# Optimization experiments

Measured on AMD Instinct MI355X. Metric: run time of the kernel, lower is better.

## Reference

```python
import jax, jax.numpy as jnp
import numpy as np

N = 50000
E = 800000
EPS = 1e-12


def sage_conv(x, src, dst, W_l, b_l, W_r):
    # PyG SAGEConv (mean aggr): out = lin_l(mean_{j in N(i)} x_j) + lin_r(x_i)
    msg = x[src]                                             # [E, d] gather
    agg = jax.ops.segment_sum(msg, dst, num_segments=N)      # [N, d]
    cnt = jax.ops.segment_sum(jnp.ones((E,), x.dtype), dst, num_segments=N)
    mean = agg / jnp.maximum(cnt, 1.0)[:, None]              # isolated nodes -> 0
    return mean @ W_l + b_l + x @ W_r


def setup_inputs() -> dict:
    key = jax.random.key(0)
    ks = jax.random.split(key, 12)
    s = 0.05
    return {
        "x": jax.random.normal(ks[0], (N, 128), dtype=jnp.float32),
        "edge_index": jax.random.randint(ks[1], (2, E), 0, N, dtype=jnp.int64),
        # pre: Linear(128 -> 128)
        "pre_W": jax.random.normal(ks[2], (128, 128), dtype=jnp.float32) * s,
        "pre_b": jnp.zeros((128,), dtype=jnp.float32),
        # conv_first: SAGEConv(128 -> 256)
        "W1_l": jax.random.normal(ks[3], (128, 256), dtype=jnp.float32) * s,
        "b1": jnp.zeros((256,), dtype=jnp.float32),
        "W1_r": jax.random.normal(ks[4], (128, 256), dtype=jnp.float32) * s,
        # conv_hidden[0]: SAGEConv(256 -> 256)
        "W2_l": jax.random.normal(ks[5], (256, 256), dtype=jnp.float32) * s,
        "b2": jnp.zeros((256,), dtype=jnp.float32),
        "W2_r": jax.random.normal(ks[6], (256, 256), dtype=jnp.float32) * s,
        # conv_out: SAGEConv(256 -> 256)
        "W3_l": jax.random.normal(ks[7], (256, 256), dtype=jnp.float32) * s,
        "b3": jnp.zeros((256,), dtype=jnp.float32),
        "W3_r": jax.random.normal(ks[8], (256, 256), dtype=jnp.float32) * s,
    }


def reference(x, edge_index, pre_W, pre_b, W1_l, b1, W1_r, W2_l, b2, W2_r, W3_l, b3, W3_r):
    src, dst = edge_index[0], edge_index[1]
    h = x @ pre_W + pre_b                                   # feature_pre Linear
    h = jax.nn.relu(sage_conv(h, src, dst, W1_l, b1, W1_r))  # dropout = identity (eval)
    h = jax.nn.relu(sage_conv(h, src, dst, W2_l, b2, W2_r))
    h = sage_conv(h, src, dst, W3_l, b3, W3_r)
    norm = jnp.sqrt(jnp.sum(h * h, axis=-1, keepdims=True))
    return h / jnp.maximum(norm, EPS)                       # F.normalize(p=2, dim=-1)
```

## Files before the change

### kernel.cpp

```cpp
#include <hip/hip_runtime.h>
#include <cstddef>
#include <cstdint>


typedef __attribute__((ext_vector_type(8))) short short8;
typedef __attribute__((ext_vector_type(4))) float f32x4;
typedef __attribute__((ext_vector_type(2))) float f32x2;

__device__ __forceinline__ unsigned rne_bf16(float f) {
    unsigned b = __float_as_uint(f);
    return (b + 0x7fffu + ((b >> 16) & 1u)) >> 16;
}
__device__ __forceinline__ float bf16_lo(unsigned u) { return __uint_as_float(u << 16); }
__device__ __forceinline__ float bf16_hi(unsigned u) { return __uint_as_float(u & 0xffff0000u); }


__device__ __forceinline__ float dec_e4m3_sw(unsigned v) {
    unsigned s = (v & 0x80u) << 24;
    unsigned em = v & 0x7fu;
    float out;
    if (em < 8u) {
        out = (float)em * 0.001953125f;
    } else {
        out = __uint_as_float((((em >> 3) + 120u) << 23) | ((em & 7u) << 20));
    }
    return __uint_as_float(__float_as_uint(out) | s);
}

__device__ __forceinline__ unsigned char enc_e4m3(float f) {
#if __has_builtin(__builtin_amdgcn_cvt_pk_fp8_f32)
    return (unsigned char)(__builtin_amdgcn_cvt_pk_fp8_f32(f, f, 0, false) & 0xff);
#else
    unsigned b = __float_as_uint(f);
    unsigned s = (b >> 24) & 0x80u;
    unsigned a = b & 0x7fffffffu;
    if (a >= 0x43E00000u) return (unsigned char)(s | 0x7Eu);
    if (a < 0x3C800000u) {
        unsigned m = (unsigned)rintf(__uint_as_float(a) * 512.0f);
        return (unsigned char)(s | m);
    }
    unsigned r = a + 0x7FFFFu + ((a >> 20) & 1u);
    unsigned E8 = (r >> 23) - 120u;
    unsigned M = (r >> 20) & 7u;
    if (E8 > 15u || (E8 == 15u && M == 7u)) return (unsigned char)(s | 0x7Eu);
    return (unsigned char)(s | (E8 << 3) | M);
#endif
}

__device__ __forceinline__ void acc16(float* a, uint4 u) {
#if __has_builtin(__builtin_amdgcn_cvt_pk_f32_fp8)
    f32x2 f;
    f = __builtin_amdgcn_cvt_pk_f32_fp8(u.x, false); a[0] += f.x;  a[1] += f.y;
    f = __builtin_amdgcn_cvt_pk_f32_fp8(u.x, true);  a[2] += f.x;  a[3] += f.y;
    f = __builtin_amdgcn_cvt_pk_f32_fp8(u.y, false); a[4] += f.x;  a[5] += f.y;
    f = __builtin_amdgcn_cvt_pk_f32_fp8(u.y, true);  a[6] += f.x;  a[7] += f.y;
    f = __builtin_amdgcn_cvt_pk_f32_fp8(u.z, false); a[8] += f.x;  a[9] += f.y;
    f = __builtin_amdgcn_cvt_pk_f32_fp8(u.z, true);  a[10] += f.x; a[11] += f.y;
    f = __builtin_amdgcn_cvt_pk_f32_fp8(u.w, false); a[12] += f.x; a[13] += f.y;
    f = __builtin_amdgcn_cvt_pk_f32_fp8(u.w, true);  a[14] += f.x; a[15] += f.y;
#else
    unsigned d0 = u.x, d1 = u.y, d2 = u.z, d3 = u.w;
#pragma unroll
    for (int t = 0; t < 4; ++t) a[t]      += dec_e4m3_sw((d0 >> (8 * t)) & 0xffu);
#pragma unroll
    for (int t = 0; t < 4; ++t) a[4 + t]  += dec_e4m3_sw((d1 >> (8 * t)) & 0xffu);
#pragma unroll
    for (int t = 0; t < 4; ++t) a[8 + t]  += dec_e4m3_sw((d2 >> (8 * t)) & 0xffu);
#pragma unroll
    for (int t = 0; t < 4; ++t) a[12 + t] += dec_e4m3_sw((d3 >> (8 * t)) & 0xffu);
#endif
}

__device__ __forceinline__ void stage16(const void* g, unsigned short* ldsbase,
                                        int lane) {
#if __has_builtin(__builtin_amdgcn_global_load_lds)
    (void)lane;
    __builtin_amdgcn_global_load_lds(
        (const __attribute__((address_space(1))) unsigned int*)g,
        (__attribute__((address_space(3))) unsigned int*)ldsbase, 16, 0, 0);
#else
    *(uint4*)(ldsbase + (size_t)lane * 8) = *(const uint4*)g;
#endif
}


__global__ __launch_bounds__(256) void deg_kernel(const int* __restrict__ dst,
                                                  int* __restrict__ deg, int E) {
    int e = blockIdx.x * 256 + threadIdx.x;
    if (e < E) atomicAdd(&deg[dst[e]], 1);
}

__global__ __launch_bounds__(256) void bsum_kernel(const int* __restrict__ deg,
                                                   int* __restrict__ bsum, int n) {
    int i = blockIdx.x * 256 + threadIdx.x;
    int v = (i < n) ? deg[i] : 0;
#pragma unroll
    for (int s = 32; s > 0; s >>= 1) v += __shfl_down(v, s);
    __shared__ int ws[4];
    int lane = threadIdx.x & 63, w = threadIdx.x >> 6;
    if (lane == 0) ws[w] = v;
    __syncthreads();
    if (threadIdx.x == 0) bsum[blockIdx.x] = ws[0] + ws[1] + ws[2] + ws[3];
}

__global__ __launch_bounds__(256) void bscan_kernel(const int* __restrict__ bsum,
                                                    int* __restrict__ boff,
                                                    int* __restrict__ off,
                                                    int nb, int n, int E) {
    int t = threadIdx.x;
    int v = (t < nb) ? bsum[t] : 0;
    int incl = v;
#pragma unroll
    for (int s = 1; s < 64; s <<= 1) {
        int u = __shfl_up(incl, s);
        if ((t & 63) >= s) incl += u;
    }
    __shared__ int ws[4];
    int lane = t & 63, w = t >> 6;
    if (lane == 63) ws[w] = incl;
    __syncthreads();
    int woff = 0;
    for (int j = 0; j < w; ++j) woff += ws[j];
    if (t < nb) boff[t] = woff + incl - v;
    if (t == 0) off[n] = E;
}

__global__ __launch_bounds__(256) void scan_kernel(const int* __restrict__ deg,
                                                   const int* __restrict__ boff,
                                                   int* __restrict__ off,
                                                   float* __restrict__ inv, int n) {
    int i = blockIdx.x * 256 + threadIdx.x;
    int v = (i < n) ? deg[i] : 0;
    int incl = v;
#pragma unroll
    for (int s = 1; s < 64; s <<= 1) {
        int u = __shfl_up(incl, s);
        if ((threadIdx.x & 63) >= s) incl += u;
    }
    __shared__ int ws[4];
    int lane = threadIdx.x & 63, w = threadIdx.x >> 6;
    if (lane == 63) ws[w] = incl;
    __syncthreads();
    int woff = 0;
    for (int j = 0; j < w; ++j) woff += ws[j];
    if (i < n) {
        off[i] = boff[blockIdx.x] + woff + incl - v;
        inv[i] = 1.0f / fmaxf((float)v, 1.0f);
    }
}

__global__ __launch_bounds__(256) void fill_kernel(const int* __restrict__ src,
                                                   const int* __restrict__ dst,
                                                   const int* __restrict__ off,
                                                   int* __restrict__ deg,
                                                   int* __restrict__ ssrc, int E) {
    int e = blockIdx.x * 256 + threadIdx.x;
    if (e >= E) return;
    int d = dst[e];
    int pos = off[d] + atomicSub(&deg[d], 1) - 1;
    ssrc[pos] = src[e];
}


__global__ __launch_bounds__(256) void prep_all(
    const float* __restrict__ x, uint2* __restrict__ xb, int n4, int XB,
    const float* __restrict__ pre_W, const float* __restrict__ W1_l,
    const float* __restrict__ W1_r, const float* __restrict__ W2_l,
    const float* __restrict__ W2_r, const float* __restrict__ W3_l,
    const float* __restrict__ W3_r,
    unsigned short* __restrict__ WT0, unsigned short* __restrict__ WT1,
    unsigned short* __restrict__ WT2, unsigned short* __restrict__ WT3,
    unsigned short* __restrict__ WT4, unsigned short* __restrict__ WT5,
    unsigned short* __restrict__ WT6) {
    if (blockIdx.x < (unsigned)XB) {
        int i = blockIdx.x * 256 + threadIdx.x;
        if (i >= n4) return;
        float4 v = ((const float4*)x)[i];
        uint2 o;
        o.x = rne_bf16(v.x) | (rne_bf16(v.y) << 16);
        o.y = rne_bf16(v.z) | (rne_bf16(v.w) << 16);
        xb[i] = o;
        return;
    }
    int idx = (blockIdx.x - XB) * 256 + threadIdx.x;
    if (idx < 16384) {
        int k = idx >> 7, n = idx & 127;
        WT0[n * 128 + k] = (unsigned short)rne_bf16(pre_W[idx]);
        return;
    }
    idx -= 16384;
    if (idx < 32768) {
        int k = idx >> 8, n = idx & 255;
        WT1[n * 128 + k] = (unsigned short)rne_bf16(W1_l[idx]);
        return;
    }
    idx -= 32768;
    if (idx < 32768) {
        int k = idx >> 8, n = idx & 255;
        WT2[n * 128 + k] = (unsigned short)rne_bf16(W1_r[idx]);
        return;
    }
    idx -= 32768;
    if (idx < 65536) {
        int k = idx >> 8, n = idx & 255;
        WT3[n * 256 + k] = (unsigned short)rne_bf16(W2_l[idx]);
        return;
    }
    idx -= 65536;
    if (idx < 65536) {
        int k = idx >> 8, n = idx & 255;
        WT4[n * 256 + k] = (unsigned short)rne_bf16(W2_r[idx]);
        return;
    }
    idx -= 65536;
    if (idx < 65536) {
        int k = idx >> 8, n = idx & 255;
        WT5[n * 256 + k] = (unsigned short)rne_bf16(W3_l[idx]);
        return;
    }
    idx -= 65536;
    if (idx < 65536) {
        int k = idx >> 8, n = idx & 255;
        WT6[n * 256 + k] = (unsigned short)rne_bf16(W3_r[idx]);
    }
}


template <int D>
__global__ __launch_bounds__(256) void gather_b(const unsigned short* __restrict__ h,
                                                const int* __restrict__ off,
                                                const int* __restrict__ ssrc,
                                                const float* __restrict__ inv,
                                                unsigned short* __restrict__ agg, int n) {
    int node = blockIdx.x * 4 + (threadIdx.x >> 6);
    if (node >= n) return;
    int lane = threadIdx.x & 63;
    int beg = off[node], end = off[node + 1];
    float sc = inv[node];

    const int q   = lane >> 4;
    const int sub = lane & 15;
    const unsigned short* col = h + (sub << 3);
    float a[8] = {0, 0, 0, 0, 0, 0, 0, 0};
    float b[8] = {0, 0, 0, 0, 0, 0, 0, 0};
    int k = beg;
    for (; k + 7 < end; k += 8) {
        int s0 = ssrc[k + q];
        int s1 = ssrc[k + 4 + q];
        uint4 u = *(const uint4*)(col + (size_t)s0 * D);
        uint4 v = *(const uint4*)(col + (size_t)s1 * D);
        a[0] += bf16_lo(u.x); a[1] += bf16_hi(u.x);
        a[2] += bf16_lo(u.y); a[3] += bf16_hi(u.y);
        a[4] += bf16_lo(u.z); a[5] += bf16_hi(u.z);
        a[6] += bf16_lo(u.w); a[7] += bf16_hi(u.w);
        b[0] += bf16_lo(v.x); b[1] += bf16_hi(v.x);
        b[2] += bf16_lo(v.y); b[3] += bf16_hi(v.y);
        b[4] += bf16_lo(v.z); b[5] += bf16_hi(v.z);
        b[6] += bf16_lo(v.w); b[7] += bf16_hi(v.w);
    }
    for (; k < end; k += 4) {
        int e = k + q;
        if (e < end) {
            uint4 u = *(const uint4*)(col + (size_t)ssrc[e] * D);
            a[0] += bf16_lo(u.x); a[1] += bf16_hi(u.x);
            a[2] += bf16_lo(u.y); a[3] += bf16_hi(u.y);
            a[4] += bf16_lo(u.z); a[5] += bf16_hi(u.z);
            a[6] += bf16_lo(u.w); a[7] += bf16_hi(u.w);
        }
    }
#pragma unroll
    for (int i = 0; i < 8; ++i) a[i] += b[i];
#pragma unroll
    for (int i = 0; i < 8; ++i) a[i] += __shfl_xor(a[i], 16);
#pragma unroll
    for (int i = 0; i < 8; ++i) a[i] += __shfl_xor(a[i], 32);
    if (q == 0) {
#pragma unroll
        for (int i = 0; i < 8; ++i) a[i] *= sc;
        uint4 o;
        o.x = rne_bf16(a[0]) | (rne_bf16(a[1]) << 16);
        o.y = rne_bf16(a[2]) | (rne_bf16(a[3]) << 16);
        o.z = rne_bf16(a[4]) | (rne_bf16(a[5]) << 16);
        o.w = rne_bf16(a[6]) | (rne_bf16(a[7]) << 16);
        *(uint4*)(agg + (size_t)node * D + (sub << 3)) = o;
    }
}


__global__ __launch_bounds__(256) void gather8(const unsigned char* __restrict__ h8,
                                               const int* __restrict__ off,
                                               const int* __restrict__ ssrc,
                                               const float* __restrict__ inv,
                                               unsigned short* __restrict__ agg, int n) {
    int node = blockIdx.x * 4 + (threadIdx.x >> 6);
    if (node >= n) return;
    int lane = threadIdx.x & 63;
    const int q   = lane >> 4;
    const int sub = lane & 15;
    int beg = off[node], end = off[node + 1];
    float sc = inv[node];
    const unsigned char* col = h8 + (sub << 4);

    float a[16], b[16];
#pragma unroll
    for (int i = 0; i < 16; ++i) { a[i] = 0.f; b[i] = 0.f; }

    int k = beg;
    for (; k + 7 < end; k += 8) {
        int s0 = ssrc[k + q];
        int s1 = ssrc[k + 4 + q];
        uint4 u = *(const uint4*)(col + (size_t)s0 * 256);
        uint4 v = *(const uint4*)(col + (size_t)s1 * 256);
        acc16(a, u);
        acc16(b, v);
    }
    for (; k < end; k += 4) {
        int e = k + q;
        if (e < end) {
            uint4 u = *(const uint4*)(col + (size_t)ssrc[e] * 256);
            acc16(a, u);
        }
    }
#pragma unroll
    for (int i = 0; i < 16; ++i) a[i] += b[i];
#pragma unroll
    for (int i = 0; i < 16; ++i) a[i] += __shfl_xor(a[i], 16);
#pragma unroll
    for (int i = 0; i < 16; ++i) a[i] += __shfl_xor(a[i], 32);
    if (q == 0) {
#pragma unroll
        for (int i = 0; i < 16; ++i) a[i] *= sc;
        uint4 o1, o2;
        o1.x = rne_bf16(a[0])  | (rne_bf16(a[1])  << 16);
        o1.y = rne_bf16(a[2])  | (rne_bf16(a[3])  << 16);
        o1.z = rne_bf16(a[4])  | (rne_bf16(a[5])  << 16);
        o1.w = rne_bf16(a[6])  | (rne_bf16(a[7])  << 16);
        o2.x = rne_bf16(a[8])  | (rne_bf16(a[9])  << 16);
        o2.y = rne_bf16(a[10]) | (rne_bf16(a[11]) << 16);
        o2.z = rne_bf16(a[12]) | (rne_bf16(a[13]) << 16);
        o2.w = rne_bf16(a[14]) | (rne_bf16(a[15]) << 16);
        *(uint4*)(agg + (size_t)node * 256 + (sub << 4)) = o1;
        *(uint4*)(agg + (size_t)node * 256 + (sub << 4) + 8) = o2;
    }
}

__global__ __launch_bounds__(256) void gemm_bt(
    const unsigned short* __restrict__ A1, const unsigned short* __restrict__ W1T,
    const float* __restrict__ bias, unsigned short* __restrict__ outb,
    int M, int K, int Nn) {
    __shared__ __align__(16) unsigned short As[128 * 64];
    __shared__ __align__(16) unsigned short Bs[128 * 64];

    const int t = threadIdx.x;
    const int lane = t & 63;
    const int w = t >> 6;
    const int wm = w >> 1, wn = w & 1;
    const int m0 = blockIdx.x * 128;
    const int n0 = blockIdx.y * 128;

    f32x4 acc[4][4];
#pragma unroll
    for (int i = 0; i < 4; ++i)
#pragma unroll
        for (int j = 0; j < 4; ++j) acc[i][j] = (f32x4){0.f, 0.f, 0.f, 0.f};

    for (int k0 = 0; k0 < K; k0 += 64) {
#pragma unroll
        for (int r = 0; r < 4; ++r) {
            int p = r * 256 + t;
            int row = p >> 3, slot = p & 7;
            int c = slot ^ (row & 7);
            int gm = m0 + row;
            if (gm >= M) gm = M - 1;
            uint4 va = *(const uint4*)(A1 + (size_t)gm * K + k0 + c * 8);
            uint4 vb = *(const uint4*)(W1T + (size_t)(n0 + row) * K + k0 + c * 8);
            *(uint4*)&As[(size_t)p * 8] = va;
            *(uint4*)&Bs[(size_t)p * 8] = vb;
        }
        __syncthreads();
#pragma unroll
        for (int kk = 0; kk < 2; ++kk) {
            short8 af[4], bfr[4];
            int ac = kk * 4 + (lane >> 4);
#pragma unroll
            for (int i = 0; i < 4; ++i) {
                int arow = wm * 64 + i * 16 + (lane & 15);
                af[i] = *(const short8*)&As[arow * 64 + ((ac ^ (arow & 7)) << 3)];
                int brow = wn * 64 + i * 16 + (lane & 15);
                bfr[i] = *(const short8*)&Bs[brow * 64 + ((ac ^ (brow & 7)) << 3)];
            }
#pragma unroll
            for (int mi = 0; mi < 4; ++mi)
#pragma unroll
                for (int ni = 0; ni < 4; ++ni)
                    acc[mi][ni] = __builtin_amdgcn_mfma_f32_16x16x32_bf16(
                        af[mi], bfr[ni], acc[mi][ni], 0, 0, 0);
        }
        __syncthreads();
    }

#pragma unroll
    for (int ni = 0; ni < 4; ++ni) {
        int n = n0 + wn * 64 + ni * 16 + (lane & 15);
        float bv = (bias != nullptr) ? bias[n] : 0.0f;
#pragma unroll
        for (int mi = 0; mi < 4; ++mi) {
            int mbase = m0 + wm * 64 + mi * 16 + ((lane >> 4) << 2);
#pragma unroll
            for (int r = 0; r < 4; ++r) {
                int m = mbase + r;
                if (m >= M) continue;
                outb[(size_t)m * Nn + n] = (unsigned short)rne_bf16(acc[mi][ni][r] + bv);
            }
        }
    }
}

__global__ __launch_bounds__(512) void gemm_wide(
    const unsigned short* __restrict__ A1, const unsigned short* __restrict__ W1T,
    const unsigned short* __restrict__ A2, const unsigned short* __restrict__ W2T,
    const float* __restrict__ bias,
    unsigned short* __restrict__ outb, unsigned char* __restrict__ out8,
    float* __restrict__ outf, int M, int K, int relu) {
    __shared__ __align__(16) unsigned short As[128 * 64];
    __shared__ __align__(16) unsigned short Bs[256 * 64];
    __shared__ float rs[128][4];

    const int t = threadIdx.x;
    const int lane = t & 63;
    const int w8 = t >> 6;
    const int wm = w8 >> 2, wn = w8 & 3;
    const int m0 = blockIdx.x * 128;

    f32x4 acc[4][4];
#pragma unroll
    for (int i = 0; i < 4; ++i)
#pragma unroll
        for (int j = 0; j < 4; ++j) acc[i][j] = (f32x4){0.f, 0.f, 0.f, 0.f};

    for (int pass = 0; pass < 2; ++pass) {
        const unsigned short* A = pass ? A2 : A1;
        const unsigned short* W = pass ? W2T : W1T;

        for (int k0 = 0; k0 < K; k0 += 64) {
#pragma unroll
            for (int i = 0; i < 2; ++i) {
                int base = (w8 * 2 + i) * 64;
                int p = base + lane;
                int row = p >> 3, slot = p & 7;
                int c = slot ^ (row & 7);
                int gm = m0 + row;
                if (gm >= M) gm = M - 1;
                stage16(A + (size_t)gm * K + k0 + c * 8, &As[(size_t)base * 8], lane);
            }
#pragma unroll
            for (int i = 0; i < 4; ++i) {
                int base = (w8 * 4 + i) * 64;
                int p = base + lane;
                int row = p >> 3, slot = p & 7;
                int c = slot ^ (row & 7);
                stage16(W + (size_t)row * K + k0 + c * 8, &Bs[(size_t)base * 8], lane);
            }
            __syncthreads();
#pragma unroll
            for (int kk = 0; kk < 2; ++kk) {
                short8 af[4], bfr[4];
                int ac = kk * 4 + (lane >> 4);
#pragma unroll
                for (int i = 0; i < 4; ++i) {
                    int arow = wm * 64 + i * 16 + (lane & 15);
                    af[i] = *(const short8*)&As[arow * 64 + ((ac ^ (arow & 7)) << 3)];
                    int brow = wn * 64 + i * 16 + (lane & 15);
                    bfr[i] = *(const short8*)&Bs[brow * 64 + ((ac ^ (brow & 7)) << 3)];
                }
#pragma unroll
                for (int mi = 0; mi < 4; ++mi)
#pragma unroll
                    for (int ni = 0; ni < 4; ++ni)
                        acc[mi][ni] = __builtin_amdgcn_mfma_f32_16x16x32_bf16(
                            af[mi], bfr[ni], acc[mi][ni], 0, 0, 0);
            }
            __syncthreads();
        }
    }

    if (outb) {
#pragma unroll
        for (int ni = 0; ni < 4; ++ni) {
            int n = wn * 64 + ni * 16 + (lane & 15);
            float bv = bias[n];
#pragma unroll
            for (int mi = 0; mi < 4; ++mi) {
                int mbase = m0 + wm * 64 + mi * 16 + ((lane >> 4) << 2);
#pragma unroll
                for (int r = 0; r < 4; ++r) {
                    int m = mbase + r;
                    if (m >= M) continue;
                    float v = acc[mi][ni][r] + bv;
                    if (relu) v = fmaxf(v, 0.0f);
                    outb[(size_t)m * 256 + n] = (unsigned short)rne_bf16(v);
                    if (out8) out8[(size_t)m * 256 + n] = enc_e4m3(v);
                }
            }
        }
        return;
    }

#pragma unroll
    for (int ni = 0; ni < 4; ++ni) {
        float bv = bias[wn * 64 + ni * 16 + (lane & 15)];
#pragma unroll
        for (int mi = 0; mi < 4; ++mi)
#pragma unroll
            for (int r = 0; r < 4; ++r) acc[mi][ni][r] += bv;
    }
#pragma unroll
    for (int mi = 0; mi < 4; ++mi) {
#pragma unroll
        for (int r = 0; r < 4; ++r) {
            float p = acc[mi][0][r] * acc[mi][0][r] + acc[mi][1][r] * acc[mi][1][r] +
                      acc[mi][2][r] * acc[mi][2][r] + acc[mi][3][r] * acc[mi][3][r];
            p += __shfl_xor(p, 1);
            p += __shfl_xor(p, 2);
            p += __shfl_xor(p, 4);
            p += __shfl_xor(p, 8);
            if ((lane & 15) == 0)
                rs[wm * 64 + mi * 16 + ((lane >> 4) << 2) + r][wn] = p;
        }
    }
    __syncthreads();
#pragma unroll
    for (int mi = 0; mi < 4; ++mi) {
        int mbase = m0 + wm * 64 + mi * 16 + ((lane >> 4) << 2);
        int lrow = wm * 64 + mi * 16 + ((lane >> 4) << 2);
#pragma unroll
        for (int r = 0; r < 4; ++r) {
            int m = mbase + r;
            if (m >= M) continue;
            float s = rs[lrow + r][0] + rs[lrow + r][1] + rs[lrow + r][2] + rs[lrow + r][3];
            float sc = 1.0f / fmaxf(sqrtf(s), 1e-12f);
#pragma unroll
            for (int ni = 0; ni < 4; ++ni) {
                int n = wn * 64 + ni * 16 + (lane & 15);
                outf[(size_t)m * 256 + n] = acc[mi][ni][r] * sc;
            }
        }
    }
}

extern "C" void kernel_launch(void* const* d_in, const int* in_sizes, int n_in,
                              void* d_out, int out_size, void* d_ws, size_t ws_size,
                              hipStream_t stream) {
    const int N = 50000;
    const int E = 800000;
    const int NB = (N + 255) / 256;

    const float* x     = (const float*)d_in[0];
    const int*   ei    = (const int*)d_in[1];
    const float* pre_W = (const float*)d_in[2];
    const float* pre_b = (const float*)d_in[3];
    const float* W1_l  = (const float*)d_in[4];
    const float* b1    = (const float*)d_in[5];
    const float* W1_r  = (const float*)d_in[6];
    const float* W2_l  = (const float*)d_in[7];
    const float* b2    = (const float*)d_in[8];
    const float* W2_r  = (const float*)d_in[9];
    const float* W3_l  = (const float*)d_in[10];
    const float* b3    = (const float*)d_in[11];
    const float* W3_r  = (const float*)d_in[12];
    float* out = (float*)d_out;

    const int* src = ei;
    const int* dst = ei + E;

    int* deg  = (int*)d_ws;
    int* off  = deg + N;
    int* bsum = off + N + 1;
    int* boff = bsum + 256;
    int* ssrc = boff + 256;
    size_t int_words = (size_t)2 * N + 1 + 512 + E;
    int_words = (int_words + 3) & ~(size_t)3;

    float* inv = (float*)d_ws + int_words;
    unsigned short* us = (unsigned short*)(inv + N);

    unsigned short* xb  = us;                 us += (size_t)N * 128;
    unsigned short* WT0 = us;                 us += 16384;
    unsigned short* WT1 = us;                 us += 32768;
    unsigned short* WT2 = us;                 us += 32768;
    unsigned short* WT3 = us;                 us += 65536;
    unsigned short* WT4 = us;                 us += 65536;
    unsigned short* WT5 = us;                 us += 65536;
    unsigned short* WT6 = us;                 us += 65536;
    unsigned short* h0b   = us;               us += (size_t)N * 128;
    unsigned short* agg1b = us;               us += (size_t)N * 128;
    unsigned short* h1b   = us;               us += (size_t)N * 256;
    unsigned short* agg2b = us;               us += (size_t)N * 256;
    unsigned short* h2b   = us;               us += (size_t)N * 256;
    unsigned short* agg3b = us;               us += (size_t)N * 256;
    unsigned char* h1f8 = (unsigned char*)us;
    unsigned char* h2f8 = h1f8 + (size_t)N * 256;

    hipMemsetAsync(deg, 0, (size_t)N * sizeof(int), stream);
    deg_kernel<<<(E + 255) / 256, 256, 0, stream>>>(dst, deg, E);
    bsum_kernel<<<NB, 256, 0, stream>>>(deg, bsum, N);
    bscan_kernel<<<1, 256, 0, stream>>>(bsum, boff, off, NB, N, E);
    scan_kernel<<<NB, 256, 0, stream>>>(deg, boff, off, inv, N);
    fill_kernel<<<(E + 255) / 256, 256, 0, stream>>>(src, dst, off, deg, ssrc, E);

    const int n4 = N * 128 / 4;
    const int XB = (n4 + 255) / 256;
    const int WB = (344064 + 255) / 256;
    prep_all<<<XB + WB, 256, 0, stream>>>(x, (uint2*)xb, n4, XB,
                                          pre_W, W1_l, W1_r, W2_l, W2_r, W3_l,
                                          W3_r, WT0, WT1, WT2, WT3, WT4, WT5, WT6);

    const int MT = (N + 127) / 128;
    const int AG = (N + 3) / 4;

    gemm_bt<<<dim3(MT, 1), 256, 0, stream>>>(xb, WT0, pre_b, h0b, N, 128, 128);

    gather_b<128><<<AG, 256, 0, stream>>>(h0b, off, ssrc, inv, agg1b, N);
    gemm_wide<<<MT, 512, 0, stream>>>(agg1b, WT1, h0b, WT2, b1,
                                      h1b, h1f8, nullptr, N, 128, 1);

    gather8<<<AG, 256, 0, stream>>>(h1f8, off, ssrc, inv, agg2b, N);
    gemm_wide<<<MT, 512, 0, stream>>>(agg2b, WT3, h1b, WT4, b2,
                                      h2b, h2f8, nullptr, N, 256, 1);

    gather8<<<AG, 256, 0, stream>>>(h2f8, off, ssrc, inv, agg3b, N);
    gemm_wide<<<MT, 512, 0, stream>>>(agg3b, WT5, h2b, WT6, b3,
                                      nullptr, nullptr, out, N, 256, 0);
}
```

Baseline: 470.4 us.

## Fuse CSR fill into pre-GEMM launch and halve gemm_wide row tile

```diff
diff --git a/kernel.cpp b/kernel.cpp
--- a/kernel.cpp
+++ b/kernel.cpp
@@ -147,18 +147,6 @@
         off[i] = boff[blockIdx.x] + woff + incl - v;
         inv[i] = 1.0f / fmaxf((float)v, 1.0f);
     }
-}
-
-__global__ __launch_bounds__(256) void fill_kernel(const int* __restrict__ src,
-                                                   const int* __restrict__ dst,
-                                                   const int* __restrict__ off,
-                                                   int* __restrict__ deg,
-                                                   int* __restrict__ ssrc, int E) {
-    int e = blockIdx.x * 256 + threadIdx.x;
-    if (e >= E) return;
-    int d = dst[e];
-    int pos = off[d] + atomicSub(&deg[d], 1) - 1;
-    ssrc[pos] = src[e];
 }
 
 
@@ -344,19 +332,32 @@
     }
 }
 
-__global__ __launch_bounds__(256) void gemm_bt(
-    const unsigned short* __restrict__ A1, const unsigned short* __restrict__ W1T,
-    const float* __restrict__ bias, unsigned short* __restrict__ outb,
-    int M, int K, int Nn) {
+
+__global__ __launch_bounds__(256) void fatB(
+    const unsigned short* __restrict__ xb, const unsigned short* __restrict__ WT0,
+    const float* __restrict__ pre_b, unsigned short* __restrict__ h0b, int M,
+    int GB,
+    const int* __restrict__ src, const int* __restrict__ dst,
+    const int* __restrict__ off, int* __restrict__ deg,
+    int* __restrict__ ssrc, int E) {
     __shared__ __align__(16) unsigned short As[128 * 64];
     __shared__ __align__(16) unsigned short Bs[128 * 64];
+
+    if (blockIdx.x >= (unsigned)GB) {
+        int e = (blockIdx.x - GB) * 256 + threadIdx.x;
+        if (e >= E) return;
+        int d = dst[e];
+        int pos = off[d] + atomicSub(&deg[d], 1) - 1;
+        ssrc[pos] = src[e];
+        return;
+    }
 
     const int t = threadIdx.x;
     const int lane = t & 63;
     const int w = t >> 6;
     const int wm = w >> 1, wn = w & 1;
     const int m0 = blockIdx.x * 128;
-    const int n0 = blockIdx.y * 128;
+    const int K = 128, Nn = 128;
 
     f32x4 acc[4][4];
 #pragma unroll
@@ -372,8 +373,8 @@
             int c = slot ^ (row & 7);
             int gm = m0 + row;
             if (gm >= M) gm = M - 1;
-            uint4 va = *(const uint4*)(A1 + (size_t)gm * K + k0 + c * 8);
-            uint4 vb = *(const uint4*)(W1T + (size_t)(n0 + row) * K + k0 + c * 8);
+            uint4 va = *(const uint4*)(xb + (size_t)gm * K + k0 + c * 8);
+            uint4 vb = *(const uint4*)(WT0 + (size_t)row * K + k0 + c * 8);
             *(uint4*)&As[(size_t)p * 8] = va;
             *(uint4*)&Bs[(size_t)p * 8] = vb;
         }
@@ -401,8 +402,8 @@
 
 #pragma unroll
     for (int ni = 0; ni < 4; ++ni) {
-        int n = n0 + wn * 64 + ni * 16 + (lane & 15);
-        float bv = (bias != nullptr) ? bias[n] : 0.0f;
+        int n = wn * 64 + ni * 16 + (lane & 15);
+        float bv = pre_b[n];
 #pragma unroll
         for (int mi = 0; mi < 4; ++mi) {
             int mbase = m0 + wm * 64 + mi * 16 + ((lane >> 4) << 2);
@@ -410,27 +411,26 @@
             for (int r = 0; r < 4; ++r) {
                 int m = mbase + r;
                 if (m >= M) continue;
-                outb[(size_t)m * Nn + n] = (unsigned short)rne_bf16(acc[mi][ni][r] + bv);
+                h0b[(size_t)m * Nn + n] = (unsigned short)rne_bf16(acc[mi][ni][r] + bv);
             }
         }
     }
 }
 
-__global__ __launch_bounds__(512) void gemm_wide(
+__global__ __launch_bounds__(256) void gemm_wide(
     const unsigned short* __restrict__ A1, const unsigned short* __restrict__ W1T,
     const unsigned short* __restrict__ A2, const unsigned short* __restrict__ W2T,
     const float* __restrict__ bias,
     unsigned short* __restrict__ outb, unsigned char* __restrict__ out8,
     float* __restrict__ outf, int M, int K, int relu) {
-    __shared__ __align__(16) unsigned short As[128 * 64];
+    __shared__ __align__(16) unsigned short As[64 * 64];
     __shared__ __align__(16) unsigned short Bs[256 * 64];
-    __shared__ float rs[128][4];
+    __shared__ float rs[64][4];
 
     const int t = threadIdx.x;
     const int lane = t & 63;
-    const int w8 = t >> 6;
-    const int wm = w8 >> 2, wn = w8 & 3;
-    const int m0 = blockIdx.x * 128;
+    const int w = t >> 6;
+    const int m0 = blockIdx.x * 64;
 
     f32x4 acc[4][4];
 #pragma unroll
@@ -445,7 +445,7 @@
         for (int k0 = 0; k0 < K; k0 += 64) {
 #pragma unroll
             for (int i = 0; i < 2; ++i) {
-                int base = (w8 * 2 + i) * 64;
+                int base = (w * 2 + i) * 64;
                 int p = base + lane;
                 int row = p >> 3, slot = p & 7;
                 int c = slot ^ (row & 7);
@@ -454,8 +454,8 @@
                 stage16(A + (size_t)gm * K + k0 + c * 8, &As[(size_t)base * 8], lane);
             }
 #pragma unroll
-            for (int i = 0; i < 4; ++i) {
-                int base = (w8 * 4 + i) * 64;
+            for (int i = 0; i < 8; ++i) {
+                int base = (w * 8 + i) * 64;
                 int p = base + lane;
                 int row = p >> 3, slot = p & 7;
                 int c = slot ^ (row & 7);
@@ -468,9 +468,9 @@
                 int ac = kk * 4 + (lane >> 4);
 #pragma unroll
                 for (int i = 0; i < 4; ++i) {
-                    int arow = wm * 64 + i * 16 + (lane & 15);
+                    int arow = i * 16 + (lane & 15);
                     af[i] = *(const short8*)&As[arow * 64 + ((ac ^ (arow & 7)) << 3)];
-                    int brow = wn * 64 + i * 16 + (lane & 15);
+                    int brow = w * 64 + i * 16 + (lane & 15);
                     bfr[i] = *(const short8*)&Bs[brow * 64 + ((ac ^ (brow & 7)) << 3)];
                 }
 #pragma unroll
@@ -487,11 +487,11 @@
     if (outb) {
 #pragma unroll
         for (int ni = 0; ni < 4; ++ni) {
-            int n = wn * 64 + ni * 16 + (lane & 15);
+            int n = w * 64 + ni * 16 + (lane & 15);
             float bv = bias[n];
 #pragma unroll
             for (int mi = 0; mi < 4; ++mi) {
-                int mbase = m0 + wm * 64 + mi * 16 + ((lane >> 4) << 2);
+                int mbase = m0 + mi * 16 + ((lane >> 4) << 2);
 #pragma unroll
                 for (int r = 0; r < 4; ++r) {
                     int m = mbase + r;
@@ -508,7 +508,7 @@
 
 #pragma unroll
     for (int ni = 0; ni < 4; ++ni) {
-        float bv = bias[wn * 64 + ni * 16 + (lane & 15)];
+        float bv = bias[w * 64 + ni * 16 + (lane & 15)];
 #pragma unroll
         for (int mi = 0; mi < 4; ++mi)
 #pragma unroll
@@ -525,23 +525,22 @@
             p += __shfl_xor(p, 4);
             p += __shfl_xor(p, 8);
             if ((lane & 15) == 0)
-                rs[wm * 64 + mi * 16 + ((lane >> 4) << 2) + r][wn] = p;
+                rs[mi * 16 + ((lane >> 4) << 2) + r][w] = p;
         }
     }
     __syncthreads();
 #pragma unroll
     for (int mi = 0; mi < 4; ++mi) {
-        int mbase = m0 + wm * 64 + mi * 16 + ((lane >> 4) << 2);
-        int lrow = wm * 64 + mi * 16 + ((lane >> 4) << 2);
+        int lrow0 = mi * 16 + ((lane >> 4) << 2);
 #pragma unroll
         for (int r = 0; r < 4; ++r) {
-            int m = mbase + r;
+            int m = m0 + lrow0 + r;
             if (m >= M) continue;
-            float s = rs[lrow + r][0] + rs[lrow + r][1] + rs[lrow + r][2] + rs[lrow + r][3];
+            float s = rs[lrow0 + r][0] + rs[lrow0 + r][1] + rs[lrow0 + r][2] + rs[lrow0 + r][3];
             float sc = 1.0f / fmaxf(sqrtf(s), 1e-12f);
 #pragma unroll
             for (int ni = 0; ni < 4; ++ni) {
-                int n = wn * 64 + ni * 16 + (lane & 15);
+                int n = w * 64 + ni * 16 + (lane & 15);
                 outf[(size_t)m * 256 + n] = acc[mi][ni][r] * sc;
             }
         }
@@ -606,7 +605,6 @@
     bsum_kernel<<<NB, 256, 0, stream>>>(deg, bsum, N);
     bscan_kernel<<<1, 256, 0, stream>>>(bsum, boff, off, NB, N, E);
     scan_kernel<<<NB, 256, 0, stream>>>(deg, boff, off, inv, N);
-    fill_kernel<<<(E + 255) / 256, 256, 0, stream>>>(src, dst, off, deg, ssrc, E);
 
     const int n4 = N * 128 / 4;
     const int XB = (n4 + 255) / 256;
@@ -616,19 +614,22 @@
                                           W3_r, WT0, WT1, WT2, WT3, WT4, WT5, WT6);
 
     const int MT = (N + 127) / 128;
+    const int MT2 = (N + 63) / 64;
     const int AG = (N + 3) / 4;
-
-    gemm_bt<<<dim3(MT, 1), 256, 0, stream>>>(xb, WT0, pre_b, h0b, N, 128, 128);
+    const int DB = (E + 255) / 256;
+
+    fatB<<<MT + DB, 256, 0, stream>>>(xb, WT0, pre_b, h0b, N, MT,
+                                      src, dst, off, deg, ssrc, E);
 
     gather_b<128><<<AG, 256, 0, stream>>>(h0b, off, ssrc, inv, agg1b, N);
-    gemm_wide<<<MT, 512, 0, stream>>>(agg1b, WT1, h0b, WT2, b1,
-                                      h1b, h1f8, nullptr, N, 128, 1);
+    gemm_wide<<<MT2, 256, 0, stream>>>(agg1b, WT1, h0b, WT2, b1,
+                                       h1b, h1f8, nullptr, N, 128, 1);
 
     gather8<<<AG, 256, 0, stream>>>(h1f8, off, ssrc, inv, agg2b, N);
-    gemm_wide<<<MT, 512, 0, stream>>>(agg2b, WT3, h1b, WT4, b2,
-                                      h2b, h2f8, nullptr, N, 256, 1);
+    gemm_wide<<<MT2, 256, 0, stream>>>(agg2b, WT3, h1b, WT4, b2,
+                                       h2b, h2f8, nullptr, N, 256, 1);
 
     gather8<<<AG, 256, 0, stream>>>(h2f8, off, ssrc, inv, agg3b, N);
-    gemm_wide<<<MT, 512, 0, stream>>>(agg3b, WT5, h2b, WT6, b3,
-                                      nullptr, nullptr, out, N, 256, 0);
-}
+    gemm_wide<<<MT2, 256, 0, stream>>>(agg3b, WT5, h2b, WT6, b3,
+                                       nullptr, nullptr, out, N, 256, 0);
+}
```

Result: no change. 461.4 us (-1.9%).
